# Kernel tuning notes

Hardware: AMD Instinct MI355X
Metric: run time of the kernel (lower is better)

The kernel has to match this reference:

```python
import jax, jax.numpy as jnp
import numpy as np
import math

B, T, L, M = 2, 16, 256, 512
D, H, DH, HT, ROT = 1024, 16, 64, 8, 32
EPS = 1e-5
NEG = jnp.float32(-1e9)
SCALE = 1.0 / math.sqrt(DH)


def _ln(x, g, b):
    mu = jnp.mean(x, -1, keepdims=True)
    var = jnp.mean((x - mu) ** 2, -1, keepdims=True)
    return (x - mu) * jax.lax.rsqrt(var + EPS) * g + b


def _rotate_half(x):
    x1, x2 = jnp.split(x, 2, axis=-1)
    return jnp.concatenate([-x2, x1], axis=-1)


def _apply_rope(t, pos):
    # t: (..., DH), pos broadcastable to (..., ROT)
    t_rot, t_pass = t[..., :ROT], t[..., ROT:]
    t_rot = t_rot * jnp.cos(pos) + _rotate_half(t_rot) * jnp.sin(pos)
    return jnp.concatenate([t_rot, t_pass], axis=-1)


def _decoder_layer(x, context, rope,
                   ca_ng, ca_nb, ca_cng, ca_cnb, ca_wq, ca_wkv, ca_wo,
                   ta_ng, ta_nb, ta_wqkv, ta_bqkv, ta_wo,
                   ff_ng, ff_nb, ff_w1, ff_w2,
                   context_mask, attn_mask):
    # ---- CrossAttention over flattened (t l) sequence ----
    xf = x.reshape(B, T * L, D)
    xn = _ln(xf, ca_ng, ca_nb)
    cn = _ln(context, ca_cng, ca_cnb)
    q = (xn @ ca_wq).reshape(B, T * L, H, DH)
    k, v = jnp.split(cn @ ca_wkv, 2, axis=-1)
    k = k.reshape(B, M, H, DH)
    v = v.reshape(B, M, H, DH)
    scores = jnp.einsum('bnhd,bmhd->bhnm', q, k) * SCALE
    scores = jnp.where(context_mask[:, None, None, :], scores, NEG)
    attn = jax.nn.softmax(scores, axis=-1)
    o = jnp.einsum('bhnm,bmhd->bnhd', attn, v).reshape(B, T * L, H * DH)
    x = x + (o @ ca_wo).reshape(B, T, L, D)

    # ---- PatchWiseTemporalAttention: attention over T at each spatial l ----
    xn = _ln(x, ta_ng, ta_nb)
    qkv = xn @ ta_wqkv + ta_bqkv  # (B,T,L,3*HT*DH)
    q, k, v = jnp.split(qkv, 3, axis=-1)
    q = q.reshape(B, T, L, HT, DH)
    k = k.reshape(B, T, L, HT, DH)
    v = v.reshape(B, T, L, HT, DH)
    # varlen rotary: masks are left-aligned so packed position == frame index t
    pos = rope[:, None, None, :]  # (T,1,1,ROT)
    q = _apply_rope(q, pos)
    k = _apply_rope(k, pos)
    scores = jnp.einsum('bqlhd,bklhd->blhqk', q, k) * SCALE
    scores = jnp.where(attn_mask[:, None, None, None, :], scores, NEG)
    attn = jax.nn.softmax(scores, axis=-1)
    o = jnp.einsum('blhqk,bklhd->bqlhd', attn, v).reshape(B, T, L, HT * DH)
    # pad_input fills zeros at invalid (masked) query rows before to_out (no bias)
    o = o * attn_mask[:, :, None, None].astype(o.dtype)
    x = x + o @ ta_wo

    # ---- FeedForward (LN -> Linear -> GELU(exact) -> Linear) ----
    h = jax.nn.gelu(_ln(x, ff_ng, ff_nb) @ ff_w1, approximate=False)
    x = x + h @ ff_w2
    return x


def setup_inputs():
    key = jax.random.key(0)
    ks = jax.random.split(key, 16)
    s = 0.02
    inner, inner_t, hid = H * DH, HT * DH, 4 * D
    lens = jax.random.randint(ks[0], (B,), 2, T + 1)
    attn_mask = jnp.arange(T)[None, :] < lens[:, None]  # left-aligned ragged lengths
    clens = jax.random.randint(ks[1], (B,), M // 2, M + 1)
    context_mask = jnp.arange(M)[None, :] < clens[:, None]
    return dict(
        x=jax.random.normal(ks[2], (B, T, L, D), jnp.float32),
        context=jax.random.normal(ks[3], (B, M, D), jnp.float32),
        rope=jax.random.normal(ks[4], (T, ROT), jnp.float32),
        ca_ng=jnp.ones((D,), jnp.float32), ca_nb=jnp.zeros((D,), jnp.float32),
        ca_cng=jnp.ones((D,), jnp.float32), ca_cnb=jnp.zeros((D,), jnp.float32),
        ca_wq=jax.random.normal(ks[5], (D, inner), jnp.float32) * s,
        ca_wkv=jax.random.normal(ks[6], (D, 2 * inner), jnp.float32) * s,
        ca_wo=jax.random.normal(ks[7], (inner, D), jnp.float32) * s,
        ta_ng=jnp.ones((D,), jnp.float32), ta_nb=jnp.zeros((D,), jnp.float32),
        ta_wqkv=jax.random.normal(ks[8], (D, 3 * inner_t), jnp.float32) * s,
        ta_bqkv=jnp.zeros((3 * inner_t,), jnp.float32),
        ta_wo=jax.random.normal(ks[9], (inner_t, D), jnp.float32) * s,
        ff_ng=jnp.ones((D,), jnp.float32), ff_nb=jnp.zeros((D,), jnp.float32),
        ff_w1=jax.random.normal(ks[10], (D, hid), jnp.float32) * s,
        ff_w2=jax.random.normal(ks[11], (hid, D), jnp.float32) * s,
        context_mask=context_mask,
        attn_mask=attn_mask,
    )


def reference(x, context, rope,
              ca_ng, ca_nb, ca_cng, ca_cnb, ca_wq, ca_wkv, ca_wo,
              ta_ng, ta_nb, ta_wqkv, ta_bqkv, ta_wo,
              ff_ng, ff_nb, ff_w1, ff_w2,
              context_mask, attn_mask):
    return _decoder_layer(x, context, rope,
                          ca_ng, ca_nb, ca_cng, ca_cnb, ca_wq, ca_wkv, ca_wo,
                          ta_ng, ta_nb, ta_wqkv, ta_bqkv, ta_wo,
                          ff_ng, ff_nb, ff_w1, ff_w2,
                          context_mask, attn_mask)
```

## Files before the change

kernel.cpp:

```cpp
#include <hip/hip_runtime.h>
#include <hip/hip_bf16.h>
#include <stdint.h>

#define DEV static __device__ __forceinline__

constexpr int kB = 2, kT = 16, kL = 256, kM = 512;
constexpr int kD = 1024, kH = 16, kDH = 64, kHT = 8, kROT = 32;
constexpr int kN = kT * kL;
constexpr float kEPS = 1e-5f;
constexpr float kNEG = -1.0e9f;
constexpr float kSCALE = 0.125f;

typedef __attribute__((ext_vector_type(8))) short short8;
typedef __attribute__((ext_vector_type(4))) float floatx4;
typedef __attribute__((ext_vector_type(16))) float floatx16;

DEV float b2f(__hip_bfloat16 v) { return __bfloat162float(v); }
DEV __hip_bfloat16 f2b(float v) { return __float2bfloat16(v); }
DEV float s2f(short x) {
  __hip_bfloat16_raw r; r.x = (unsigned short)x;
  return __bfloat162float(__hip_bfloat16(r));
}

DEV void gl2lds16(const __hip_bfloat16* g, __hip_bfloat16* l) {
  __builtin_amdgcn_global_load_lds(
      (const __attribute__((address_space(1))) void*)g,
      (__attribute__((address_space(3))) void*)l, 16, 0, 0);
}

struct TransArgs {
  const float* src[7];
  __hip_bfloat16* dst[7];
  const unsigned char* cmraw;
  const unsigned char* amraw;
  int* cmask;
  int* amask;
};
__constant__ const int kTKd[7] = {1024, 1024, 1024, 1024, 512, 1024, 4096};
__constant__ const int kTNd[7] = {1024, 2048, 1024, 1536, 1024, 4096, 1024};
__constant__ const int kTCum[8] = {0, 1024, 3072, 4096, 5632, 6144, 10240, 14336};

DEV int mask_val(const unsigned char* raw, int i) {
  unsigned char b1 = raw[1], b3 = raw[3];
  if (b1 == 0x3F) return ((const unsigned short*)raw)[i] != 0;
  if (b3 == 0x3F) return ((const float*)raw)[i] != 0.0f;
  if (b1 == 1)    return raw[i] != 0;
  return ((const int*)raw)[i] != 0;
}

__global__ __launch_bounds__(256) void transpose_all(TransArgs a) {
  int id = blockIdx.x;
  if (id >= 14336) {
    if (id == 14336) {
      for (int i = threadIdx.x; i < kB * kM; i += 256)
        a.cmask[i] = mask_val(a.cmraw, i);
    } else {
      if (threadIdx.x < kB * kT)
        a.amask[threadIdx.x] = mask_val(a.amraw, threadIdx.x);
    }
    return;
  }
  int seg = 0;
  #pragma unroll
  for (int s = 1; s < 7; s++) seg += (id >= kTCum[s]);
  unsigned t = id - kTCum[seg];
  int Kd = kTKd[seg], Nd = kTNd[seg];
  unsigned ntx = Nd / 32;
  int n0 = (t % ntx) * 32, k0 = (t / ntx) * 32;
  const float* W = a.src[seg];
  __hip_bfloat16* Wt = a.dst[seg];
  __shared__ float tile[32][33];
  int tx = threadIdx.x & 31, ty = threadIdx.x >> 5;
  for (int i = 0; i < 32; i += 8)
    tile[ty + i][tx] = W[(size_t)(k0 + ty + i) * Nd + n0 + tx];
  __syncthreads();
  for (int i = 0; i < 32; i += 8)
    Wt[(size_t)(n0 + ty + i) * Kd + k0 + tx] = f2b(tile[tx][ty + i]);
}

DEV void ln_body(const float* xr, const float* g, const float* bb,
                 __hip_bfloat16* outr, int tid) {
  float4 xv = *(const float4*)(xr + tid * 4);
  float s = xv.x + xv.y + xv.z + xv.w;
  float s2 = xv.x * xv.x + xv.y * xv.y + xv.z * xv.z + xv.w * xv.w;
  for (int off = 32; off; off >>= 1) {
    s += __shfl_down(s, off);
    s2 += __shfl_down(s2, off);
  }
  __shared__ float rs[4], rs2[4];
  if ((tid & 63) == 0) { rs[tid >> 6] = s; rs2[tid >> 6] = s2; }
  __syncthreads();
  float ts = rs[0] + rs[1] + rs[2] + rs[3];
  float ts2 = rs2[0] + rs2[1] + rs2[2] + rs2[3];
  float mu = ts * (1.f / kD);
  float var = ts2 * (1.f / kD) - mu * mu;
  float rstd = rsqrtf(var + kEPS);
  float4 gv = *(const float4*)(g + tid * 4);
  float4 bv = *(const float4*)(bb + tid * 4);
  ushort4 o;
  o.x = __hip_bfloat16_raw(f2b((xv.x - mu) * rstd * gv.x + bv.x)).x;
  o.y = __hip_bfloat16_raw(f2b((xv.y - mu) * rstd * gv.y + bv.y)).x;
  o.z = __hip_bfloat16_raw(f2b((xv.z - mu) * rstd * gv.z + bv.z)).x;
  o.w = __hip_bfloat16_raw(f2b((xv.w - mu) * rstd * gv.w + bv.w)).x;
  *(ushort4*)(outr + tid * 4) = o;
}

__global__ __launch_bounds__(256) void ln_rows(
    const float* __restrict__ X, const float* __restrict__ g,
    const float* __restrict__ bb, __hip_bfloat16* __restrict__ out) {
  int row = blockIdx.x;
  ln_body(X + (size_t)row * kD, g, bb, out + (size_t)row * kD, threadIdx.x);
}

__global__ __launch_bounds__(256) void ln_rows2(
    const float* __restrict__ X, const float* __restrict__ g,
    const float* __restrict__ bb, __hip_bfloat16* __restrict__ out,
    const float* __restrict__ X2, const float* __restrict__ g2,
    const float* __restrict__ bb2, __hip_bfloat16* __restrict__ out2) {
  int row = blockIdx.x;
  if (row < 8192)
    ln_body(X + (size_t)row * kD, g, bb, out + (size_t)row * kD, threadIdx.x);
  else {
    int r = row - 8192;
    ln_body(X2 + (size_t)r * kD, g2, bb2, out2 + (size_t)r * kD, threadIdx.x);
  }
}

DEV void gemm_epilogue(floatx16 acc[2][2], const float* bias, const float* res,
                       int gelu, void* out, int outBf16, int Nd,
                       int m0, int n0, int wm, int wn, int l32, int kg) {
  #pragma unroll
  for (int fa = 0; fa < 2; fa++) {
    #pragma unroll
    for (int fb = 0; fb < 2; fb++) {
      int col = n0 + wn + fb * 32 + l32;
      float bv = bias ? bias[col] : 0.f;
      #pragma unroll
      for (int r = 0; r < 16; r++) {
        int row = m0 + wm + fa * 32 + (r & 3) + 8 * (r >> 2) + 4 * kg;
        float v = acc[fa][fb][r] + bv;
        if (gelu) {
          v = v * (1.f / (1.f + __expf(-1.702f * v)));
        }
        size_t o = (size_t)row * Nd + col;
        if (res) v += res[o];
        if (outBf16) ((__hip_bfloat16*)out)[o] = f2b(v);
        else         ((float*)out)[o] = v;
      }
    }
  }
}

DEV void gemm_body(__hip_bfloat16* As, __hip_bfloat16* Bs,
                   const __hip_bfloat16* A, const __hip_bfloat16* Bt,
                   const float* bias, const float* res, int gelu,
                   void* out, int outBf16, int Nd, int Kd, int m0, int n0) {
  int tid = threadIdx.x, wave = tid >> 6, lane = tid & 63;
  int l32 = lane & 31, kg = lane >> 5;
  int wm = (wave >> 1) * 64, wn = (wave & 1) * 64;

  int srow = wave * 32 + (lane >> 3);
  int schunk8 = (((lane & 7) ^ ((lane >> 3) & 7)) << 3);
  const __hip_bfloat16* Ag = A + (size_t)(m0 + srow) * Kd + schunk8;
  const __hip_bfloat16* Bg = Bt + (size_t)(n0 + srow) * Kd + schunk8;
  __hip_bfloat16* Al = As + wave * 32 * 64;
  __hip_bfloat16* Bl = Bs + wave * 32 * 64;

  floatx16 acc[2][2] = {};
  for (int k0 = 0; k0 < Kd; k0 += 64) {
    #pragma unroll
    for (int i = 0; i < 4; i++) {
      gl2lds16(Ag + (size_t)(i * 8) * Kd + k0, Al + i * 512);
      gl2lds16(Bg + (size_t)(i * 8) * Kd + k0, Bl + i * 512);
    }
    __syncthreads();
    #pragma unroll
    for (int ks = 0; ks < 4; ks++) {
      int c = ks * 2 + kg;
      short8 af[2], bf2[2];
      #pragma unroll
      for (int fa = 0; fa < 2; fa++) {
        int row = wm + fa * 32 + l32;
        af[fa] = *(const short8*)(&As[row * 64 + (c ^ (row & 7)) * 8]);
      }
      #pragma unroll
      for (int fb = 0; fb < 2; fb++) {
        int row = wn + fb * 32 + l32;
        bf2[fb] = *(const short8*)(&Bs[row * 64 + (c ^ (row & 7)) * 8]);
      }
      #pragma unroll
      for (int fa = 0; fa < 2; fa++)
        #pragma unroll
        for (int fb = 0; fb < 2; fb++)
          acc[fa][fb] = __builtin_amdgcn_mfma_f32_32x32x16_bf16(
              af[fa], bf2[fb], acc[fa][fb], 0, 0, 0);
    }
    __syncthreads();
  }
  gemm_epilogue(acc, bias, res, gelu, out, outBf16, Nd, m0, n0, wm, wn, l32, kg);
}

__global__ __launch_bounds__(256) void gemm_bf16(
    const __hip_bfloat16* __restrict__ A, const __hip_bfloat16* __restrict__ Bt,
    const float* __restrict__ bias, const float* __restrict__ res, int gelu,
    void* __restrict__ out, int outBf16, int Nd, int Kd) {
  __shared__ __align__(16) __hip_bfloat16 As[128 * 64];
  __shared__ __align__(16) __hip_bfloat16 Bs[128 * 64];
  gemm_body(As, Bs, A, Bt, bias, res, gelu, out, outBf16, Nd, Kd,
            blockIdx.x * 128, blockIdx.y * 128);
}

__global__ __launch_bounds__(512, 2) void gemm_pipe(
    const __hip_bfloat16* __restrict__ A, const __hip_bfloat16* __restrict__ Bt,
    const float* __restrict__ bias, const float* __restrict__ res, int gelu,
    void* __restrict__ out, int outBf16, int Nd, int Kd) {
  __shared__ __align__(16) __hip_bfloat16 As[4][128 * 32];
  __shared__ __align__(16) __hip_bfloat16 Bs[4][256 * 32];
  const int m0 = blockIdx.x * 128, n0 = blockIdx.y * 256;
  const int tid = threadIdx.x, wave = tid >> 6, lane = tid & 63;
  const int l32 = lane & 31, kg = lane >> 5;
  const int wm = (wave >> 2) * 64, wn = (wave & 3) * 64;
  const int NT = Kd >> 5;

  const int arow = wave * 16 + (lane >> 2);
  const int alc = (lane & 3) ^ ((arow >> 1) & 3);
  const __hip_bfloat16* Ag = A + (size_t)(m0 + arow) * Kd + alc * 8;
  const int brow0 = wave * 32 + (lane >> 2);
  const int brow1 = brow0 + 16;
  const int blc0 = (lane & 3) ^ ((brow0 >> 1) & 3);
  const int blc1 = (lane & 3) ^ ((brow1 >> 1) & 3);
  const __hip_bfloat16* Bg0 = Bt + (size_t)(n0 + brow0) * Kd + blc0 * 8;
  const __hip_bfloat16* Bg1 = Bt + (size_t)(n0 + brow1) * Kd + blc1 * 8;
  __hip_bfloat16* Al = &As[0][0] + wave * 512;
  __hip_bfloat16* Bl0 = &Bs[0][0] + wave * 1024;
  __hip_bfloat16* Bl1 = Bl0 + 512;

  auto stage = [&](int t) {
    int slot = t & 3, k0 = t << 5;
    gl2lds16(Ag + k0, Al + slot * 4096);
    gl2lds16(Bg0 + k0, Bl0 + slot * 8192);
    gl2lds16(Bg1 + k0, Bl1 + slot * 8192);
  };

  floatx16 acc[2][2] = {};

  stage(0); stage(1); stage(2);
  asm volatile("s_waitcnt vmcnt(6)" ::: "memory");
  __builtin_amdgcn_s_barrier();
  asm volatile("" ::: "memory");

  for (int t = 0; t < NT; ++t) {
    const __hip_bfloat16* Asl = &As[t & 3][0];
    const __hip_bfloat16* Bsl = &Bs[t & 3][0];
    short8 af[2][2], bf2[2][2];
    #pragma unroll
    for (int ks = 0; ks < 2; ks++) {
      int c = ks * 2 + kg;
      #pragma unroll
      for (int fa = 0; fa < 2; fa++) {
        int row = wm + fa * 32 + l32;
        af[ks][fa] = *(const short8*)(Asl + row * 32 + (c ^ ((row >> 1) & 3)) * 8);
      }
      #pragma unroll
      for (int fb = 0; fb < 2; fb++) {
        int row = wn + fb * 32 + l32;
        bf2[ks][fb] = *(const short8*)(Bsl + row * 32 + (c ^ ((row >> 1) & 3)) * 8);
      }
    }
    if (t + 3 < NT) stage(t + 3);
    __builtin_amdgcn_s_barrier();
    asm volatile("s_waitcnt lgkmcnt(0)" ::: "memory");
    __builtin_amdgcn_s_setprio(1);
    #pragma unroll
    for (int ks = 0; ks < 2; ks++)
      #pragma unroll
      for (int fa = 0; fa < 2; fa++)
        #pragma unroll
        for (int fb = 0; fb < 2; fb++)
          acc[fa][fb] = __builtin_amdgcn_mfma_f32_32x32x16_bf16(
              af[ks][fa], bf2[ks][fb], acc[fa][fb], 0, 0, 0);
    __builtin_amdgcn_s_setprio(0);
    if (t < NT - 3)       asm volatile("s_waitcnt vmcnt(6)" ::: "memory");
    else if (t == NT - 3) asm volatile("s_waitcnt vmcnt(3)" ::: "memory");
    else if (t == NT - 2) asm volatile("s_waitcnt vmcnt(0)" ::: "memory");
    __builtin_amdgcn_s_barrier();
    asm volatile("" ::: "memory");
    __builtin_amdgcn_sched_barrier(0);
  }

  gemm_epilogue(acc, bias, res, gelu, out, outBf16, Nd, m0, n0, wm, wn, l32, kg);
}

__global__ __launch_bounds__(256) void cross_attn_mfma(
    const __hip_bfloat16* __restrict__ Qb,
    const __hip_bfloat16* __restrict__ KVb,
    const int* __restrict__ cmask,
    __hip_bfloat16* __restrict__ Ob) {
  __shared__ __align__(16) __hip_bfloat16 Vbf[2][8][64][8];
  __shared__ __align__(16) __hip_bfloat16 Paf[4][8][16][8];
  int b = blockIdx.y >> 4, h = blockIdx.y & 15;
  int q0 = blockIdx.x * 64;
  int tid = threadIdx.x, wave = tid >> 6, lane = tid & 63;
  int l16 = lane & 15, quad = lane >> 4;

  const __hip_bfloat16* qrow =
      Qb + (size_t)(b * kN + q0 + wave * 16 + l16) * 1024 + h * 64 + quad * 8;
  short8 qf0 = *(const short8*)qrow;
  short8 qf1 = *(const short8*)(qrow + 32);

  floatx4 of[4] = {};
  float Mr[4] = {-1e30f, -1e30f, -1e30f, -1e30f};
  float Lr[4] = {};

  int skey = tid >> 2, sd0 = (tid & 3) * 16;

  for (int kt = 0; kt < 8; kt++) {
    int buf = kt & 1;
    {
      const __hip_bfloat16* src =
          KVb + (size_t)(b * kM + kt * 64 + skey) * 2048 + 1024 + h * 64 + sd0;
      short8 v0 = *(const short8*)src;
      short8 v1 = *(const short8*)(src + 8);
      int kb = skey >> 3, kj = skey & 7;
      #pragma unroll
      for (int j = 0; j < 8; j++) {
        Vbf[buf][kb][sd0 + j][kj] = __hip_bfloat16(__hip_bfloat16_raw{(unsigned short)v0[j]});
        Vbf[buf][kb][sd0 + 8 + j][kj] = __hip_bfloat16(__hip_bfloat16_raw{(unsigned short)v1[j]});
      }
    }
    __syncthreads();

    floatx4 sf[4];
    #pragma unroll
    for (int nf = 0; nf < 4; nf++) {
      const __hip_bfloat16* krow =
          KVb + (size_t)(b * kM + kt * 64 + nf * 16 + l16) * 2048 + h * 64 + quad * 8;
      short8 kf0 = *(const short8*)krow;
      short8 kf1 = *(const short8*)(krow + 32);
      floatx4 z = {};
      z = __builtin_amdgcn_mfma_f32_16x16x32_bf16(qf0, kf0, z, 0, 0, 0);
      z = __builtin_amdgcn_mfma_f32_16x16x32_bf16(qf1, kf1, z, 0, 0, 0);
      sf[nf] = z;
    }

    float sv[4][4];
    #pragma unroll
    for (int nf = 0; nf < 4; nf++) {
      int mk = cmask[b * kM + kt * 64 + nf * 16 + l16];
      #pragma unroll
      for (int r = 0; r < 4; r++)
        sv[nf][r] = mk ? sf[nf][r] * kSCALE : kNEG;
    }
    float mx[4];
    #pragma unroll
    for (int r = 0; r < 4; r++) {
      float m = fmaxf(fmaxf(sv[0][r], sv[1][r]), fmaxf(sv[2][r], sv[3][r]));
      #pragma unroll
      for (int off = 1; off < 16; off <<= 1) m = fmaxf(m, __shfl_xor(m, off));
      mx[r] = m;
    }
    float alpha[4], Mn[4];
    #pragma unroll
    for (int r = 0; r < 4; r++) {
      Mn[r] = fmaxf(Mr[r], mx[r]);
      alpha[r] = __expf(Mr[r] - Mn[r]);
      Mr[r] = Mn[r];
    }
    float p[4][4];
    float rsum[4];
    #pragma unroll
    for (int r = 0; r < 4; r++) {
      float s = 0.f;
      #pragma unroll
      for (int nf = 0; nf < 4; nf++) {
        float e = __expf(sv[nf][r] - Mn[r]);
        p[nf][r] = e; s += e;
      }
      #pragma unroll
      for (int off = 1; off < 16; off <<= 1) s += __shfl_xor(s, off);
      rsum[r] = s;
    }
    #pragma unroll
    for (int r = 0; r < 4; r++) Lr[r] = Lr[r] * alpha[r] + rsum[r];
    #pragma unroll
    for (int df = 0; df < 4; df++)
      #pragma unroll
      for (int r = 0; r < 4; r++) of[df][r] *= alpha[r];

    #pragma unroll
    for (int nf = 0; nf < 4; nf++) {
      int col = nf * 16 + l16;
      int kb = col >> 3, kj = col & 7;
      #pragma unroll
      for (int r = 0; r < 4; r++)
        Paf[wave][kb][quad * 4 + r][kj] = f2b(p[nf][r]);
    }
    __builtin_amdgcn_s_waitcnt(0);

    short8 pf0 = *(const short8*)(&Paf[wave][quad][l16][0]);
    short8 pf1 = *(const short8*)(&Paf[wave][quad + 4][l16][0]);
    #pragma unroll
    for (int df = 0; df < 4; df++) {
      short8 vf0 = *(const short8*)(&Vbf[buf][quad][df * 16 + l16][0]);
      short8 vf1 = *(const short8*)(&Vbf[buf][quad + 4][df * 16 + l16][0]);
      of[df] = __builtin_amdgcn_mfma_f32_16x16x32_bf16(pf0, vf0, of[df], 0, 0, 0);
      of[df] = __builtin_amdgcn_mfma_f32_16x16x32_bf16(pf1, vf1, of[df], 0, 0, 0);
    }
  }

  #pragma unroll
  for (int df = 0; df < 4; df++) {
    #pragma unroll
    for (int r = 0; r < 4; r++) {
      int row = q0 + wave * 16 + quad * 4 + r;
      float v = of[df][r] / Lr[r];
      Ob[(size_t)(b * kN + row) * 1024 + h * 64 + df * 16 + l16] = f2b(v);
    }
  }
}

__global__ __launch_bounds__(64) void temporal_attn(
    const __hip_bfloat16* __restrict__ QKVb,
    const float* __restrict__ rope,
    const int* __restrict__ amask,
    __hip_bfloat16* __restrict__ Otb) {
  __shared__ float qs[16][65], ks[16][65], vs[16][65];
  __shared__ float Ps[16][17];
  int idx = blockIdx.x;
  int h = idx & 7, l = (idx >> 3) & 255, b = idx >> 11;
  int lane = threadIdx.x;

  {
    int tr = lane >> 2, c0 = (lane & 3) * 16;
    const __hip_bfloat16* base =
        QKVb + ((size_t)(b * kT + tr) * kL + l) * 1536 + h * 64;
    short8 qa = *(const short8*)(base + c0);
    short8 qb = *(const short8*)(base + c0 + 8);
    short8 ka = *(const short8*)(base + 512 + c0);
    short8 kb = *(const short8*)(base + 512 + c0 + 8);
    short8 va = *(const short8*)(base + 1024 + c0);
    short8 vb = *(const short8*)(base + 1024 + c0 + 8);
    #pragma unroll
    for (int j = 0; j < 8; j++) {
      qs[tr][c0 + j] = s2f(qa[j]) * kSCALE;
      qs[tr][c0 + 8 + j] = s2f(qb[j]) * kSCALE;
      ks[tr][c0 + j] = s2f(ka[j]);
      ks[tr][c0 + 8 + j] = s2f(kb[j]);
      vs[tr][c0 + j] = s2f(va[j]);
      vs[tr][c0 + 8 + j] = s2f(vb[j]);
    }
  }
  __syncthreads();
  {
    int rt = lane >> 2, rd0 = (lane & 3) * 8;
    float nq[8], nk[8];
    for (int j = 0; j < 8; j++) {
      int d = rd0 + j;
      float ang = rope[rt * kROT + d];
      float cv = cosf(ang), sv = sinf(ang);
      float oq = (d < 16) ? -qs[rt][d + 16] : qs[rt][d - 16];
      float ok = (d < 16) ? -ks[rt][d + 16] : ks[rt][d - 16];
      nq[j] = qs[rt][d] * cv + oq * sv;
      nk[j] = ks[rt][d] * cv + ok * sv;
    }
    __syncthreads();
    for (int j = 0; j < 8; j++) { qs[rt][rd0 + j] = nq[j]; ks[rt][rd0 + j] = nk[j]; }
  }
  __syncthreads();
  {
    int tq = lane >> 2, tk0 = (lane & 3) * 4;
    float s[4] = {0, 0, 0, 0};
    for (int d = 0; d < 64; d++) {
      float qv = qs[tq][d];
      s[0] += qv * ks[tk0 + 0][d];
      s[1] += qv * ks[tk0 + 1][d];
      s[2] += qv * ks[tk0 + 2][d];
      s[3] += qv * ks[tk0 + 3][d];
    }
    for (int jj = 0; jj < 4; jj++)
      Ps[tq][tk0 + jj] = amask[b * kT + tk0 + jj] ? s[jj] : kNEG;
  }
  __syncthreads();
  if (lane < 16) {
    float mx = -1e30f;
    for (int k = 0; k < 16; k++) mx = fmaxf(mx, Ps[lane][k]);
    float sum = 0.f;
    for (int k = 0; k < 16; k++) { float p = __expf(Ps[lane][k] - mx); Ps[lane][k] = p; sum += p; }
    float inv = 1.f / sum;
    for (int k = 0; k < 16; k++) Ps[lane][k] *= inv;
  }
  __syncthreads();
  for (int tq = 0; tq < 16; tq++) {
    float acc = 0.f;
    for (int tk = 0; tk < 16; tk++) acc += Ps[tq][tk] * vs[tk][lane];
    float qm = amask[b * kT + tq] ? 1.f : 0.f;
    Otb[((size_t)(b * kT + tq) * kL + l) * 512 + h * 64 + lane] = f2b(acc * qm);
  }
}

extern "C" void kernel_launch(void* const* d_in, const int* in_sizes, int n_in,
                              void* d_out, int out_size, void* d_ws, size_t ws_size,
                              hipStream_t stream) {
  const float* x       = (const float*)d_in[0];
  const float* ctx     = (const float*)d_in[1];
  const float* rope    = (const float*)d_in[2];
  const float* ca_ng   = (const float*)d_in[3];
  const float* ca_nb   = (const float*)d_in[4];
  const float* ca_cng  = (const float*)d_in[5];
  const float* ca_cnb  = (const float*)d_in[6];
  const float* ca_wq   = (const float*)d_in[7];
  const float* ca_wkv  = (const float*)d_in[8];
  const float* ca_wo   = (const float*)d_in[9];
  const float* ta_ng   = (const float*)d_in[10];
  const float* ta_nb   = (const float*)d_in[11];
  const float* ta_wqkv = (const float*)d_in[12];
  const float* ta_bqkv = (const float*)d_in[13];
  const float* ta_wo   = (const float*)d_in[14];
  const float* ff_ng   = (const float*)d_in[15];
  const float* ff_nb   = (const float*)d_in[16];
  const float* ff_w1   = (const float*)d_in[17];
  const float* ff_w2   = (const float*)d_in[18];
  const unsigned char* cmraw = (const unsigned char*)d_in[19];
  const unsigned char* amraw = (const unsigned char*)d_in[20];

  char* wsc = (char*)d_ws;
  size_t off = 0;
  auto take = [&](size_t bytes) {
    char* p = wsc + off;
    off = (off + bytes + 255) & ~(size_t)255;
    return p;
  };
  __hip_bfloat16* wqT   = (__hip_bfloat16*)take((size_t)1024 * 1024 * 2);
  __hip_bfloat16* wkvT  = (__hip_bfloat16*)take((size_t)2048 * 1024 * 2);
  __hip_bfloat16* woT   = (__hip_bfloat16*)take((size_t)1024 * 1024 * 2);
  __hip_bfloat16* wqkvT = (__hip_bfloat16*)take((size_t)1536 * 1024 * 2);
  __hip_bfloat16* tawoT = (__hip_bfloat16*)take((size_t)1024 * 512 * 2);
  __hip_bfloat16* ffw1T = (__hip_bfloat16*)take((size_t)4096 * 1024 * 2);
  __hip_bfloat16* ffw2T = (__hip_bfloat16*)take((size_t)1024 * 4096 * 2);
  __hip_bfloat16* XN  = (__hip_bfloat16*)take((size_t)8192 * 1024 * 2);
  __hip_bfloat16* CN  = (__hip_bfloat16*)take((size_t)1024 * 1024 * 2);
  __hip_bfloat16* Qb  = (__hip_bfloat16*)take((size_t)8192 * 1024 * 2);
  __hip_bfloat16* KVb = (__hip_bfloat16*)take((size_t)1024 * 2048 * 2);
  __hip_bfloat16* Ob  = (__hip_bfloat16*)take((size_t)8192 * 1024 * 2);
  float*          X1  = (float*)take((size_t)8192 * 1024 * 4);
  __hip_bfloat16* Hb  = (__hip_bfloat16*)take((size_t)8192 * 4096 * 2);
  int* cmask = (int*)take((size_t)kB * kM * 4);
  int* amask = (int*)take((size_t)kB * kT * 4);
  if (off > ws_size) return;

  __hip_bfloat16* QKVb = Hb;
  __hip_bfloat16* OTb  = Qb;

  auto gemmP = [&](const __hip_bfloat16* A, const __hip_bfloat16* Bt,
                   const float* bias, const float* res, int gelu, void* out,
                   int outBf16, int Md, int Nd, int Kd) {
    gemm_pipe<<<dim3(Md / 128, Nd / 256), dim3(512), 0, stream>>>(
        A, Bt, bias, res, gelu, out, outBf16, Nd, Kd);
  };

  TransArgs ta;
  ta.src[0] = ca_wq;   ta.dst[0] = wqT;
  ta.src[1] = ca_wkv;  ta.dst[1] = wkvT;
  ta.src[2] = ca_wo;   ta.dst[2] = woT;
  ta.src[3] = ta_wqkv; ta.dst[3] = wqkvT;
  ta.src[4] = ta_wo;   ta.dst[4] = tawoT;
  ta.src[5] = ff_w1;   ta.dst[5] = ffw1T;
  ta.src[6] = ff_w2;   ta.dst[6] = ffw2T;
  ta.cmraw = cmraw; ta.amraw = amraw; ta.cmask = cmask; ta.amask = amask;
  transpose_all<<<dim3(14338), dim3(256), 0, stream>>>(ta);

  ln_rows2<<<dim3(9216), dim3(256), 0, stream>>>(x, ca_ng, ca_nb, XN,
                                                 ctx, ca_cng, ca_cnb, CN);
  gemmP(XN, wqT, nullptr, nullptr, 0, Qb, 1, 8192, 1024, 1024);
  gemm_bf16<<<dim3(8, 16), dim3(256), 0, stream>>>(
      CN, wkvT, nullptr, nullptr, 0, KVb, 1, 2048, 1024);
  cross_attn_mfma<<<dim3(kN / 64, kB * kH), dim3(256), 0, stream>>>(Qb, KVb, cmask, Ob);
  gemmP(Ob, woT, nullptr, x, 0, X1, 0, 8192, 1024, 1024);

  ln_rows<<<dim3(8192), dim3(256), 0, stream>>>(X1, ta_ng, ta_nb, XN);
  gemmP(XN, wqkvT, ta_bqkv, nullptr, 0, QKVb, 1, 8192, 1536, 1024);
  temporal_attn<<<dim3(kB * kL * kHT), dim3(64), 0, stream>>>(QKVb, rope, amask, OTb);
  gemmP(OTb, tawoT, nullptr, X1, 0, X1, 0, 8192, 1024, 512);

  ln_rows<<<dim3(8192), dim3(256), 0, stream>>>(X1, ff_ng, ff_nb, XN);
  gemmP(XN, ffw1T, nullptr, nullptr, 1, Hb, 1, 8192, 4096, 1024);
  gemmP(Hb, ffw2T, nullptr, X1, 0, d_out, 0, 8192, 1024, 4096);
}
```

Before: 683.1 us.

## Replace pipelined GEMM with simple 16x16 MFMA GEMM and fuse Q/KV projections

Removes the multi-stage pipelined 128x256 GEMM kernel and routes every projection through a simpler single-buffered 128x128 GEMM. That GEMM now uses 16x16x32 MFMA with 4x4 fragments per wave in place of 32x32x16 with 2x2, and has a matching epilogue. The cross-attention Q and KV projections are merged into a single paired launch. The loss of the 4-stage prefetch and setprio scheduling means global loads are no longer overlapped with compute, which may hurt the large FFN GEMMs.

```diff
diff --git a/kernel.cpp b/kernel.cpp
--- a/kernel.cpp
+++ b/kernel.cpp
@@ -126,19 +126,63 @@
   }
 }
 
-DEV void gemm_epilogue(floatx16 acc[2][2], const float* bias, const float* res,
-                       int gelu, void* out, int outBf16, int Nd,
-                       int m0, int n0, int wm, int wn, int l32, int kg) {
+DEV void gemm_body(__hip_bfloat16* As, __hip_bfloat16* Bs,
+                   const __hip_bfloat16* A, const __hip_bfloat16* Bt,
+                   const float* bias, const float* res, int gelu,
+                   void* out, int outBf16, int Nd, int Kd, int m0, int n0) {
+  int tid = threadIdx.x, wave = tid >> 6, lane = tid & 63;
+  int l16 = lane & 15, quad = lane >> 4;
+  int wm = (wave >> 1) * 64, wn = (wave & 1) * 64;
+
+  int srow = wave * 32 + (lane >> 3);
+  int schunk8 = (((lane & 7) ^ ((lane >> 3) & 7)) << 3);
+  const __hip_bfloat16* Ag = A + (size_t)(m0 + srow) * Kd + schunk8;
+  const __hip_bfloat16* Bg = Bt + (size_t)(n0 + srow) * Kd + schunk8;
+  __hip_bfloat16* Al = As + wave * 32 * 64;
+  __hip_bfloat16* Bl = Bs + wave * 32 * 64;
+
+  floatx4 acc[4][4] = {};
+  for (int k0 = 0; k0 < Kd; k0 += 64) {
+    #pragma unroll
+    for (int i = 0; i < 4; i++) {
+      gl2lds16(Ag + (size_t)(i * 8) * Kd + k0, Al + i * 512);
+      gl2lds16(Bg + (size_t)(i * 8) * Kd + k0, Bl + i * 512);
+    }
+    __syncthreads();
+    #pragma unroll
+    for (int ks = 0; ks < 2; ks++) {
+      short8 af[4], bf[4];
+      #pragma unroll
+      for (int mf = 0; mf < 4; mf++) {
+        int row = wm + mf * 16 + l16;
+        int c = ks * 4 + quad;
+        af[mf] = *(const short8*)(&As[row * 64 + ((c ^ (row & 7)) << 3)]);
+      }
+      #pragma unroll
+      for (int nf = 0; nf < 4; nf++) {
+        int row = wn + nf * 16 + l16;
+        int c = ks * 4 + quad;
+        bf[nf] = *(const short8*)(&Bs[row * 64 + ((c ^ (row & 7)) << 3)]);
+      }
+      #pragma unroll
+      for (int mf = 0; mf < 4; mf++)
+        #pragma unroll
+        for (int nf = 0; nf < 4; nf++)
+          acc[mf][nf] = __builtin_amdgcn_mfma_f32_16x16x32_bf16(
+              af[mf], bf[nf], acc[mf][nf], 0, 0, 0);
+    }
+    __syncthreads();
+  }
   #pragma unroll
-  for (int fa = 0; fa < 2; fa++) {
-    #pragma unroll
-    for (int fb = 0; fb < 2; fb++) {
-      int col = n0 + wn + fb * 32 + l32;
+  for (int mf = 0; mf < 4; mf++) {
+    #pragma unroll
+    for (int nf = 0; nf < 4; nf++) {
+      int col = n0 + wn + nf * 16 + l16;
       float bv = bias ? bias[col] : 0.f;
       #pragma unroll
-      for (int r = 0; r < 16; r++) {
-        int row = m0 + wm + fa * 32 + (r & 3) + 8 * (r >> 2) + 4 * kg;
-        float v = acc[fa][fb][r] + bv;
+      for (int r = 0; r < 4; r++) {
+        int row = m0 + wm + mf * 16 + quad * 4 + r;
+        float v = acc[mf][nf][r] + bv;
         if (gelu) {
           v = v * (1.f / (1.f + __expf(-1.702f * v)));
         }
@@ -151,55 +195,6 @@
   }
 }
 
-DEV void gemm_body(__hip_bfloat16* As, __hip_bfloat16* Bs,
-                   const __hip_bfloat16* A, const __hip_bfloat16* Bt,
-                   const float* bias, const float* res, int gelu,
-                   void* out, int outBf16, int Nd, int Kd, int m0, int n0) {
-  int tid = threadIdx.x, wave = tid >> 6, lane = tid & 63;
-  int l32 = lane & 31, kg = lane >> 5;
-  int wm = (wave >> 1) * 64, wn = (wave & 1) * 64;
-
-  int srow = wave * 32 + (lane >> 3);
-  int schunk8 = (((lane & 7) ^ ((lane >> 3) & 7)) << 3);
-  const __hip_bfloat16* Ag = A + (size_t)(m0 + srow) * Kd + schunk8;
-  const __hip_bfloat16* Bg = Bt + (size_t)(n0 + srow) * Kd + schunk8;
-  __hip_bfloat16* Al = As + wave * 32 * 64;
-  __hip_bfloat16* Bl = Bs + wave * 32 * 64;
-
-  floatx16 acc[2][2] = {};
-  for (int k0 = 0; k0 < Kd; k0 += 64) {
-    #pragma unroll
-    for (int i = 0; i < 4; i++) {
-      gl2lds16(Ag + (size_t)(i * 8) * Kd + k0, Al + i * 512);
-      gl2lds16(Bg + (size_t)(i * 8) * Kd + k0, Bl + i * 512);
-    }
-    __syncthreads();
-    #pragma unroll
-    for (int ks = 0; ks < 4; ks++) {
-      int c = ks * 2 + kg;
-      short8 af[2], bf2[2];
-      #pragma unroll
-      for (int fa = 0; fa < 2; fa++) {
-        int row = wm + fa * 32 + l32;
-        af[fa] = *(const short8*)(&As[row * 64 + (c ^ (row & 7)) * 8]);
-      }
-      #pragma unroll
-      for (int fb = 0; fb < 2; fb++) {
-        int row = wn + fb * 32 + l32;
-        bf2[fb] = *(const short8*)(&Bs[row * 64 + (c ^ (row & 7)) * 8]);
-      }
-      #pragma unroll
-      for (int fa = 0; fa < 2; fa++)
-        #pragma unroll
-        for (int fb = 0; fb < 2; fb++)
-          acc[fa][fb] = __builtin_amdgcn_mfma_f32_32x32x16_bf16(
-              af[fa], bf2[fb], acc[fa][fb], 0, 0, 0);
-    }
-    __syncthreads();
-  }
-  gemm_epilogue(acc, bias, res, gelu, out, outBf16, Nd, m0, n0, wm, wn, l32, kg);
-}
-
 __global__ __launch_bounds__(256) void gemm_bf16(
     const __hip_bfloat16* __restrict__ A, const __hip_bfloat16* __restrict__ Bt,
     const float* __restrict__ bias, const float* __restrict__ res, int gelu,
@@ -210,85 +205,22 @@
             blockIdx.x * 128, blockIdx.y * 128);
 }
 
-__global__ __launch_bounds__(512, 2) void gemm_pipe(
-    const __hip_bfloat16* __restrict__ A, const __hip_bfloat16* __restrict__ Bt,
-    const float* __restrict__ bias, const float* __restrict__ res, int gelu,
-    void* __restrict__ out, int outBf16, int Nd, int Kd) {
-  __shared__ __align__(16) __hip_bfloat16 As[4][128 * 32];
-  __shared__ __align__(16) __hip_bfloat16 Bs[4][256 * 32];
-  const int m0 = blockIdx.x * 128, n0 = blockIdx.y * 256;
-  const int tid = threadIdx.x, wave = tid >> 6, lane = tid & 63;
-  const int l32 = lane & 31, kg = lane >> 5;
-  const int wm = (wave >> 2) * 64, wn = (wave & 3) * 64;
-  const int NT = Kd >> 5;
-
-  const int arow = wave * 16 + (lane >> 2);
-  const int alc = (lane & 3) ^ ((arow >> 1) & 3);
-  const __hip_bfloat16* Ag = A + (size_t)(m0 + arow) * Kd + alc * 8;
-  const int brow0 = wave * 32 + (lane >> 2);
-  const int brow1 = brow0 + 16;
-  const int blc0 = (lane & 3) ^ ((brow0 >> 1) & 3);
-  const int blc1 = (lane & 3) ^ ((brow1 >> 1) & 3);
-  const __hip_bfloat16* Bg0 = Bt + (size_t)(n0 + brow0) * Kd + blc0 * 8;
-  const __hip_bfloat16* Bg1 = Bt + (size_t)(n0 + brow1) * Kd + blc1 * 8;
-  __hip_bfloat16* Al = &As[0][0] + wave * 512;
-  __hip_bfloat16* Bl0 = &Bs[0][0] + wave * 1024;
-  __hip_bfloat16* Bl1 = Bl0 + 512;
-
-  auto stage = [&](int t) {
-    int slot = t & 3, k0 = t << 5;
-    gl2lds16(Ag + k0, Al + slot * 4096);
-    gl2lds16(Bg0 + k0, Bl0 + slot * 8192);
-    gl2lds16(Bg1 + k0, Bl1 + slot * 8192);
-  };
-
-  floatx16 acc[2][2] = {};
-
-  stage(0); stage(1); stage(2);
-  asm volatile("s_waitcnt vmcnt(6)" ::: "memory");
-  __builtin_amdgcn_s_barrier();
-  asm volatile("" ::: "memory");
-
-  for (int t = 0; t < NT; ++t) {
-    const __hip_bfloat16* Asl = &As[t & 3][0];
-    const __hip_bfloat16* Bsl = &Bs[t & 3][0];
-    short8 af[2][2], bf2[2][2];
-    #pragma unroll
-    for (int ks = 0; ks < 2; ks++) {
-      int c = ks * 2 + kg;
-      #pragma unroll
-      for (int fa = 0; fa < 2; fa++) {
-        int row = wm + fa * 32 + l32;
-        af[ks][fa] = *(const short8*)(Asl + row * 32 + (c ^ ((row >> 1) & 3)) * 8);
-      }
-      #pragma unroll
-      for (int fb = 0; fb < 2; fb++) {
-        int row = wn + fb * 32 + l32;
-        bf2[ks][fb] = *(const short8*)(Bsl + row * 32 + (c ^ ((row >> 1) & 3)) * 8);
-      }
-    }
-    if (t + 3 < NT) stage(t + 3);
-    __builtin_amdgcn_s_barrier();
-    asm volatile("s_waitcnt lgkmcnt(0)" ::: "memory");
-    __builtin_amdgcn_s_setprio(1);
-    #pragma unroll
-    for (int ks = 0; ks < 2; ks++)
-      #pragma unroll
-      for (int fa = 0; fa < 2; fa++)
-        #pragma unroll
-        for (int fb = 0; fb < 2; fb++)
-          acc[fa][fb] = __builtin_amdgcn_mfma_f32_32x32x16_bf16(
-              af[ks][fa], bf2[ks][fb], acc[fa][fb], 0, 0, 0);
-    __builtin_amdgcn_s_setprio(0);
-    if (t < NT - 3)       asm volatile("s_waitcnt vmcnt(6)" ::: "memory");
-    else if (t == NT - 3) asm volatile("s_waitcnt vmcnt(3)" ::: "memory");
-    else if (t == NT - 2) asm volatile("s_waitcnt vmcnt(0)" ::: "memory");
-    __builtin_amdgcn_s_barrier();
-    asm volatile("" ::: "memory");
-    __builtin_amdgcn_sched_barrier(0);
-  }
-
-  gemm_epilogue(acc, bias, res, gelu, out, outBf16, Nd, m0, n0, wm, wn, l32, kg);
+__global__ __launch_bounds__(256) void gemm_pair(
+    const __hip_bfloat16* __restrict__ A0, const __hip_bfloat16* __restrict__ B0,
+    void* __restrict__ o0,
+    const __hip_bfloat16* __restrict__ A1, const __hip_bfloat16* __restrict__ B1,
+    void* __restrict__ o1) {
+  __shared__ __align__(16) __hip_bfloat16 As[128 * 64];
+  __shared__ __align__(16) __hip_bfloat16 Bs[128 * 64];
+  int id = blockIdx.x;
+  if (id < 512) {
+    gemm_body(As, Bs, A0, B0, nullptr, nullptr, 0, o0, 1, 1024, 1024,
+              (id & 63) * 128, (id >> 6) * 128);
+  } else {
+    int r = id - 512;
+    gemm_body(As, Bs, A1, B1, nullptr, nullptr, 0, o1, 1, 2048, 1024,
+              (r & 7) * 128, (r >> 3) * 128);
+  }
 }
 
 __global__ __launch_bounds__(256) void cross_attn_mfma(
@@ -551,10 +483,10 @@
   __hip_bfloat16* QKVb = Hb;
   __hip_bfloat16* OTb  = Qb;
 
-  auto gemmP = [&](const __hip_bfloat16* A, const __hip_bfloat16* Bt,
-                   const float* bias, const float* res, int gelu, void* out,
-                   int outBf16, int Md, int Nd, int Kd) {
-    gemm_pipe<<<dim3(Md / 128, Nd / 256), dim3(512), 0, stream>>>(
+  auto gemm = [&](const __hip_bfloat16* A, const __hip_bfloat16* Bt,
+                  const float* bias, const float* res, int gelu, void* out,
+                  int outBf16, int Md, int Nd, int Kd) {
+    gemm_bf16<<<dim3(Md / 128, Nd / 128), dim3(256), 0, stream>>>(
         A, Bt, bias, res, gelu, out, outBf16, Nd, Kd);
   };
 
@@ -571,18 +503,16 @@
 
   ln_rows2<<<dim3(9216), dim3(256), 0, stream>>>(x, ca_ng, ca_nb, XN,
                                                  ctx, ca_cng, ca_cnb, CN);
-  gemmP(XN, wqT, nullptr, nullptr, 0, Qb, 1, 8192, 1024, 1024);
-  gemm_bf16<<<dim3(8, 16), dim3(256), 0, stream>>>(
-      CN, wkvT, nullptr, nullptr, 0, KVb, 1, 2048, 1024);
+  gemm_pair<<<dim3(640), dim3(256), 0, stream>>>(XN, wqT, Qb, CN, wkvT, KVb);
   cross_attn_mfma<<<dim3(kN / 64, kB * kH), dim3(256), 0, stream>>>(Qb, KVb, cmask, Ob);
-  gemmP(Ob, woT, nullptr, x, 0, X1, 0, 8192, 1024, 1024);
+  gemm(Ob, woT, nullptr, x, 0, X1, 0, 8192, 1024, 1024);
 
   ln_rows<<<dim3(8192), dim3(256), 0, stream>>>(X1, ta_ng, ta_nb, XN);
-  gemmP(XN, wqkvT, ta_bqkv, nullptr, 0, QKVb, 1, 8192, 1536, 1024);
+  gemm(XN, wqkvT, ta_bqkv, nullptr, 0, QKVb, 1, 8192, 1536, 1024);
   temporal_attn<<<dim3(kB * kL * kHT), dim3(64), 0, stream>>>(QKVb, rope, amask, OTb);
-  gemmP(OTb, tawoT, nullptr, X1, 0, X1, 0, 8192, 1024, 512);
+  gemm(OTb, tawoT, nullptr, X1, 0, X1, 0, 8192, 1024, 512);
 
   ln_rows<<<dim3(8192), dim3(256), 0, stream>>>(X1, ff_ng, ff_nb, XN);
-  gemmP(XN, ffw1T, nullptr, nullptr, 1, Hb, 1, 8192, 4096, 1024);
-  gemmP(Hb, ffw2T, nullptr, X1, 0, d_out, 0, 8192, 1024, 4096);
-}
+  gemm(XN, ffw1T, nullptr, nullptr, 1, Hb, 1, 8192, 4096, 1024);
+  gemm(Hb, ffw2T, nullptr, X1, 0, d_out, 0, 8192, 1024, 4096);
+}
```

New measurement: 656.5 us. 1.04x faster.
